# Optimization experiments

Measured on AMD Instinct MI355X. Metric: run time of the kernel, lower is better.

Reference implementation:

```python
import jax, jax.numpy as jnp
import numpy as np
from jax import lax


def _binarize(t):
    # sign binarization to +1/-1 (zero maps to -1, matching torch.where(t > 0, 1, -1))
    return jnp.where(t > 0, 1.0, -1.0).astype(t.dtype)


def _bconv(x, w, b):
    # binary conv: binarize input and weights, then standard 3x3 'same' conv
    y = lax.conv_general_dilated(
        _binarize(x), _binarize(w),
        window_strides=(1, 1), padding=((1, 1), (1, 1)),
        dimension_numbers=('NCHW', 'OIHW', 'NCHW'))
    return y + b[None, :, None, None]


def _maxpool2(x):
    return lax.reduce_window(x, -jnp.inf, lax.max, (1, 1, 2, 2), (1, 1, 2, 2), 'VALID')


def setup_inputs() -> dict:
    key = jax.random.key(0)
    ks = jax.random.split(key, 13)
    s = 0.1
    return {
        'x': jax.random.normal(ks[0], (4096, 1, 28, 28), jnp.float32),
        'w1': jax.random.normal(ks[1], (32, 1, 3, 3), jnp.float32) * s,
        'b1': jax.random.normal(ks[2], (32,), jnp.float32) * s,
        'w2': jax.random.normal(ks[3], (64, 32, 3, 3), jnp.float32) * s,
        'b2': jax.random.normal(ks[4], (64,), jnp.float32) * s,
        'w3': jax.random.normal(ks[5], (16, 64, 3, 3), jnp.float32) * s,
        'b3': jax.random.normal(ks[6], (16,), jnp.float32) * s,
        'fc1_w': jax.random.normal(ks[7], (256, 16 * 7 * 7), jnp.float32) * s,
        'fc1_b': jax.random.normal(ks[8], (256,), jnp.float32) * s,
        'fc2_w': jax.random.normal(ks[9], (128, 256), jnp.float32) * s,
        'fc2_b': jax.random.normal(ks[10], (128,), jnp.float32) * s,
        'fc3_w': jax.random.normal(ks[11], (10, 128), jnp.float32) * s,
        'fc3_b': jax.random.normal(ks[12], (10,), jnp.float32) * s,
    }


def reference(x, w1, b1, w2, b2, w3, b3, fc1_w, fc1_b, fc2_w, fc2_b, fc3_w, fc3_b):
    h = jax.nn.relu(_maxpool2(_bconv(x, w1, b1)))      # [B,32,14,14]
    h = jax.nn.relu(_maxpool2(_bconv(h, w2, b2)))      # [B,64,7,7]
    h = jax.nn.relu(_bconv(h, w3, b3))                 # [B,16,7,7]
    h = h.reshape(-1, 16 * 7 * 7)
    h = jax.nn.relu(h @ fc1_w.T + fc1_b)
    h = jax.nn.relu(h @ fc2_w.T + fc2_b)
    return h @ fc3_w.T + fc3_b                          # [B,10]
```

## Files before the change

kernel.cpp:

```cpp
#include <hip/hip_runtime.h>
#include <cstdint>

#define OFF_W1T   4096
#define OFF_W2T   823296
#define OFF_H3T   954368
#define OFF_H1T   14061568
#define OFF_H2T   18255872

#define TW_WB1    0
#define TW_W2     32
#define TW_W3     608
#define TW_CORR2  896
#define TW_CORR3  1920
#define TW_TLE1   2176
#define TW_TGE1   2208
#define TW_TLE2   2240
#define TW_TGE2   2304

__device__ __forceinline__ int imin2(int a, int b) { return a < b ? a : b; }
__device__ __forceinline__ int imax2(int a, int b) { return a > b ? a : b; }

__device__ __forceinline__ void gload16(const float* g, float* lbase, int lane) {
#if __has_builtin(__builtin_amdgcn_global_load_lds)
    __builtin_amdgcn_global_load_lds(
        (const __attribute__((address_space(1))) uint32_t*)g,
        (__attribute__((address_space(3))) uint32_t*)lbase, 16, 0, 0);
#else
    *(float4*)&lbase[lane * 4] = *(const float4*)g;
#endif
}

__global__ __launch_bounds__(256) void prep(
    const float* __restrict__ w1, const float* __restrict__ b1,
    const float* __restrict__ w2, const float* __restrict__ b2,
    const float* __restrict__ w3,
    const float* __restrict__ fc1_w, const float* __restrict__ fc2_w,
    int* __restrict__ tab, float* __restrict__ w1T, float* __restrict__ w2T) {
    int t = threadIdx.x;
    uint32_t* utab = (uint32_t*)tab;
    if (blockIdx.x == 0) {
        if (t < 32) {
            uint32_t b = 0;
            for (int k = 0; k < 9; ++k) b |= (w1[t * 9 + k] > 0.f ? 1u : 0u) << k;
            utab[TW_WB1 + t] = b;
            tab[TW_TLE1 + t] = (int)floorf((9.f + b1[t]) * 0.5f);
            tab[TW_TGE1 + t] = (int)floorf(-b1[t]) + 1;
        }
        if (t >= 32 && t < 96) {
            int oc = t - 32;
            tab[TW_TLE2 + oc] = (int)floorf((288.f + b2[oc]) * 0.5f);
            tab[TW_TGE2 + oc] = (int)floorf(-b2[oc]) + 1;
        }
        for (int idx = t; idx < 576; idx += 256) {
            int oc = idx / 9, tap = idx % 9;
            int kh = tap / 3, kw = tap % 3;
            uint32_t b = 0;
            for (int ic = 0; ic < 32; ++ic)
                b |= (w2[((oc * 32 + ic) * 3 + kh) * 3 + kw] > 0.f ? 1u : 0u) << ic;
            utab[TW_W2 + idx] = b;
        }
        for (int idx = t; idx < 288; idx += 256) {
            int oc = idx / 18, rem = idx % 18;
            int tap = rem >> 1, word = rem & 1;
            int kh = tap / 3, kw = tap % 3;
            uint32_t b = 0;
            for (int ic = 0; ic < 32; ++ic)
                b |= (w3[((oc * 64 + ic + 32 * word) * 3 + kh) * 3 + kw] > 0.f ? 1u : 0u) << ic;
            utab[TW_W3 + idx] = b;
        }
        __syncthreads();
        for (int idx = t; idx < 1024; idx += 256) {
            int pat = idx >> 6, oc = idx & 63;
            int s = 0, n = 0;
            for (int tap = 0; tap < 9; ++tap) {
                int kh = tap / 3, kw = tap % 3;
                bool pad = ((pat & 1) && kh == 0) || ((pat & 2) && kh == 2) ||
                           ((pat & 4) && kw == 0) || ((pat & 8) && kw == 2);
                if (pad) { s += __popc(utab[TW_W2 + oc * 9 + tap]); ++n; }
            }
            tab[TW_CORR2 + idx] = 2 * s - 32 * n;
        }
        {
            int idx = t;
            if (idx < 256) {
                int pat = idx >> 4, oc = idx & 15;
                int s = 0, n = 0;
                for (int tap = 0; tap < 9; ++tap) {
                    int kh = tap / 3, kw = tap % 3;
                    bool pad = ((pat & 1) && kh == 0) || ((pat & 2) && kh == 2) ||
                               ((pat & 4) && kw == 0) || ((pat & 8) && kw == 2);
                    if (pad) {
                        s += __popc(utab[TW_W3 + oc * 18 + tap * 2]) +
                             __popc(utab[TW_W3 + oc * 18 + tap * 2 + 1]);
                        ++n;
                    }
                }
                tab[TW_CORR3 + idx] = 2 * s - 64 * n;
            }
        }
    } else {
        int e = (blockIdx.x - 1) * 256 + t;
        if (e < 204800) {
            int k = e >> 8, n = e & 255;
            w1T[e] = (k < 784) ? fc1_w[n * 784 + k] : 0.f;
        } else {
            int e2 = e - 204800;
            int k = e2 >> 7, n = e2 & 127;
            w2T[e2] = fc2_w[n * 256 + k];
        }
    }
}

#define WV 456

__global__ __launch_bounds__(512, 8) void conv_stack(
    const float* __restrict__ x,
    const float* __restrict__ b3,
    const int* __restrict__ tab,
    float* __restrict__ h3T) {
    __shared__ int SH[1280 + 4 * WV];
    const int t = threadIdx.x;
    const int wid = t >> 6, lane = t & 63;
    const int iml = wid >> 1, sw = wid & 1;
    const int img = blockIdx.x * 4 + iml;
    const uint32_t* utab = (const uint32_t*)tab;
    uint32_t* W = (uint32_t*)&SH[1280 + iml * WV];

    for (int i = t; i < 1280; i += 512) SH[i] = tab[TW_CORR2 + i];
    for (int i = t; i < 4 * WV; i += 512) SH[1280 + i] = 0;
    __syncthreads();

    if (lane < 14) {
        int r = sw * 14 + lane;
        const float* xr = x + img * 784 + r * 28;
        uint32_t b = 0;
#pragma unroll
        for (int q = 0; q < 7; ++q) {
            float4 v = *(const float4*)(xr + q * 4);
            b |= (v.x > 0.f ? 1u : 0u) << (q * 4 + 0);
            b |= (v.y > 0.f ? 1u : 0u) << (q * 4 + 1);
            b |= (v.z > 0.f ? 1u : 0u) << (q * 4 + 2);
            b |= (v.w > 0.f ? 1u : 0u) << (q * 4 + 3);
        }
        W[1 + r] = b << 1;
    }
    __syncthreads();

    auto conv1_int = [&](int p) {
        int Pi = 1 + p / 12, Pj = 1 + p % 12;
        int i0 = 2 * Pi, j0 = 2 * Pj;
        uint32_t r0 = W[i0], r1 = W[i0 + 1], r2 = W[i0 + 2], r3 = W[i0 + 3];
        uint32_t f0a = (r0 >> j0) & 7, f0b = (r0 >> (j0 + 1)) & 7;
        uint32_t f1a = (r1 >> j0) & 7, f1b = (r1 >> (j0 + 1)) & 7;
        uint32_t f2a = (r2 >> j0) & 7, f2b = (r2 >> (j0 + 1)) & 7;
        uint32_t f3a = (r3 >> j0) & 7, f3b = (r3 >> (j0 + 1)) & 7;
        uint32_t s00 = f0a | (f1a << 3) | (f2a << 6);
        uint32_t s01 = f0b | (f1b << 3) | (f2b << 6);
        uint32_t s10 = f1a | (f2a << 3) | (f3a << 6);
        uint32_t s11 = f1b | (f2b << 3) | (f3b << 6);
        uint32_t word = 0;
#pragma unroll
        for (int oc = 0; oc < 32; ++oc) {
            uint32_t w = utab[TW_WB1 + oc];
            int m0 = __popc(s00 ^ w), m1 = __popc(s01 ^ w);
            int m2 = __popc(s10 ^ w), m3 = __popc(s11 ^ w);
            int mn = imin2(imin2(m0, m1), imin2(m2, m3));
            word |= (mn <= tab[TW_TLE1 + oc] ? 1u : 0u) << oc;
        }
        W[32 + (Pi + 1) * 16 + (Pj + 1)] = word;
    };
    if (sw == 0) {
        conv1_int(lane);
        conv1_int(64 + lane);
    } else {
        if (lane < 16) conv1_int(128 + lane);
        int p = lane;
        bool act = p < 52;
        int pp = act ? p : 28;
        int Pi, Pj;
        if (pp < 14)      { Pi = 0;  Pj = pp; }
        else if (pp < 28) { Pi = 13; Pj = pp - 14; }
        else if (pp < 40) { Pi = pp - 28 + 1; Pj = 0; }
        else              { Pi = pp - 40 + 1; Pj = 13; }
        int i0 = 2 * Pi, j0 = 2 * Pj;
        uint32_t r0 = W[i0], r1 = W[i0 + 1], r2 = W[i0 + 2], r3 = W[i0 + 3];
        uint32_t f0a = (r0 >> j0) & 7, f0b = (r0 >> (j0 + 1)) & 7;
        uint32_t f1a = (r1 >> j0) & 7, f1b = (r1 >> (j0 + 1)) & 7;
        uint32_t f2a = (r2 >> j0) & 7, f2b = (r2 >> (j0 + 1)) & 7;
        uint32_t f3a = (r3 >> j0) & 7, f3b = (r3 >> (j0 + 1)) & 7;
        uint32_t smp[4];
        smp[0] = f0a | (f1a << 3) | (f2a << 6);
        smp[1] = f0b | (f1b << 3) | (f2b << 6);
        smp[2] = f1a | (f2a << 3) | (f3a << 6);
        smp[3] = f1b | (f2b << 3) | (f3b << 6);
        uint32_t mb[4];
        int pcm[4];
#pragma unroll
        for (int a = 0; a < 2; ++a) {
            int i = 2 * Pi + a;
            uint32_t vre = 0x1FF;
            if (i == 0)  vre &= ~0x007u;
            if (i == 27) vre &= ~0x1C0u;
#pragma unroll
            for (int bb = 0; bb < 2; ++bb) {
                int j = 2 * Pj + bb;
                uint32_t vce = 0x1FF;
                if (j == 0)  vce &= ~0x049u;
                if (j == 27) vce &= ~0x124u;
                mb[a * 2 + bb] = vre & vce;
                pcm[a * 2 + bb] = __popc(vre & vce);
            }
        }
        uint32_t word = 0;
#pragma unroll
        for (int oc = 0; oc < 32; ++oc) {
            uint32_t w = utab[TW_WB1 + oc];
            int best = -1000;
#pragma unroll
            for (int p4 = 0; p4 < 4; ++p4) {
                int v = pcm[p4] - 2 * __popc((smp[p4] ^ w) & mb[p4]);
                best = imax2(best, v);
            }
            word |= (best >= tab[TW_TGE1 + oc] ? 1u : 0u) << oc;
        }
        if (act) W[32 + (Pi + 1) * 16 + (Pj + 1)] = word;
    }
    __syncthreads();

    {
        uint32_t w2r[9];
#pragma unroll
        for (int k = 0; k < 9; ++k) w2r[k] = utab[TW_W2 + lane * 9 + k];
        const int tle2 = tab[TW_TLE2 + lane];
        const int tge2 = tab[TW_TGE2 + lane];
        const uint32_t* H1 = W + 32;
        uint32_t* H2 = W + 288;

        for (int q = sw; q < 25; q += 2) {
            int Pi = 1 + q / 5, Pj = 1 + q % 5;
            uint32_t c[16];
#pragma unroll
            for (int r = 0; r < 4; ++r) {
                uint2 lo = *(const uint2*)&H1[(2 * Pi + r) * 16 + 2 * Pj];
                uint2 hi = *(const uint2*)&H1[(2 * Pi + r) * 16 + 2 * Pj + 2];
                c[r * 4 + 0] = lo.x; c[r * 4 + 1] = lo.y;
                c[r * 4 + 2] = hi.x; c[r * 4 + 3] = hi.y;
            }
            int mn = 100000;
#pragma unroll
            for (int a = 0; a < 2; ++a)
#pragma unroll
                for (int bb = 0; bb < 2; ++bb) {
                    int s = 0;
#pragma unroll
                    for (int kh = 0; kh < 3; ++kh)
#pragma unroll
                        for (int kw = 0; kw < 3; ++kw)
                            s += __popc(c[(a + kh) * 4 + (bb + kw)] ^ w2r[kh * 3 + kw]);
                    mn = imin2(mn, s);
                }
            uint64_t bal = __ballot(mn <= tle2);
            if (lane == 0) {
                uint2 wv = make_uint2((uint32_t)bal, (uint32_t)(bal >> 32));
                *(uint2*)&H2[((Pi + 1) * 9 + (Pj + 1)) * 2] = wv;
            }
        }
        for (int bp = sw; bp < 24; bp += 2) {
            int Pi, Pj;
            if (bp < 7)       { Pi = 0; Pj = bp; }
            else if (bp < 14) { Pi = 6; Pj = bp - 7; }
            else if (bp < 19) { Pi = bp - 14 + 1; Pj = 0; }
            else              { Pi = bp - 19 + 1; Pj = 6; }
            uint32_t c[16];
#pragma unroll
            for (int r = 0; r < 4; ++r) {
                uint2 lo = *(const uint2*)&H1[(2 * Pi + r) * 16 + 2 * Pj];
                uint2 hi = *(const uint2*)&H1[(2 * Pi + r) * 16 + 2 * Pj + 2];
                c[r * 4 + 0] = lo.x; c[r * 4 + 1] = lo.y;
                c[r * 4 + 2] = hi.x; c[r * 4 + 3] = hi.y;
            }
            int best = -100000;
#pragma unroll
            for (int a = 0; a < 2; ++a)
#pragma unroll
                for (int bb = 0; bb < 2; ++bb) {
                    int s = 0;
#pragma unroll
                    for (int kh = 0; kh < 3; ++kh)
#pragma unroll
                        for (int kw = 0; kw < 3; ++kw)
                            s += __popc(c[(a + kh) * 4 + (bb + kw)] ^ w2r[kh * 3 + kw]);
                    int i = 2 * Pi + a, j = 2 * Pj + bb;
                    int pat = (i == 0 ? 1 : 0) | (i == 13 ? 2 : 0) |
                              (j == 0 ? 4 : 0) | (j == 13 ? 8 : 0);
                    int D = 288 - 2 * s + SH[pat * 64 + lane];
                    best = imax2(best, D);
                }
            uint64_t bal = __ballot(best >= tge2);
            if (lane == 0) {
                uint2 wv = make_uint2((uint32_t)bal, (uint32_t)(bal >> 32));
                *(uint2*)&H2[((Pi + 1) * 9 + (Pj + 1)) * 2] = wv;
            }
        }
    }
    __syncthreads();

    {
        const uint32_t* H2 = (const uint32_t*)W + 288;
        int oc = lane & 15, sub = lane >> 4;
        uint32_t w3r[18];
#pragma unroll
        for (int k = 0; k < 18; ++k) w3r[k] = utab[TW_W3 + oc * 18 + k];
        float bias3 = b3[oc];
        const int gbeg = sw ? 6 : 0, gend = sw ? 13 : 6;
        for (int g = gbeg; g < gend; ++g) {
            int pos = g * 4 + sub;
            bool act = pos < 49;
            int pp = act ? pos : 0;
            int Pi = pp / 7, Pj = pp % 7;
            int s = 0;
#pragma unroll
            for (int kh = 0; kh < 3; ++kh)
#pragma unroll
                for (int kw = 0; kw < 3; ++kw) {
                    uint2 hv = *(const uint2*)&H2[((Pi + kh) * 9 + (Pj + kw)) * 2];
                    s += __popc(hv.x ^ w3r[(kh * 3 + kw) * 2]) +
                         __popc(hv.y ^ w3r[(kh * 3 + kw) * 2 + 1]);
                }
            int pat = (Pi == 0 ? 1 : 0) | (Pi == 6 ? 2 : 0) |
                      (Pj == 0 ? 4 : 0) | (Pj == 6 ? 8 : 0);
            int D = 576 - 2 * s + SH[1024 + pat * 16 + oc];
            float h = (float)D + bias3;
            h = h > 0.f ? h : 0.f;
            if (act) h3T[(oc * 49 + pp) * 4096 + img] = h;
        }
    }
}

__global__ __launch_bounds__(256) void fc1_gemm(
    const float* __restrict__ aT,
    const float* __restrict__ bT,
    const float* __restrict__ bias,
    float* __restrict__ oT) {
    const int KC = 40;
    __shared__ float As[2][KC * 64];
    __shared__ float Bs[2][KC * 64];
    const int t = threadIdx.x;
    const int lane = t & 63, wid = t >> 6;
    const int tx = t & 15, ty = t >> 4;
    const int img0 = blockIdx.x * 64;
    const int n0 = blockIdx.y * 64;
    float acc[4][4] = {{0.f}};

    auto stage = [&](int buf, int kc) {
        for (int s = wid; s < 20; s += 4) {
            int seg = s < 10 ? s : s - 10;
            int kk = seg * 4 + (lane >> 4);
            int c = (lane & 15) * 4;
            if (s < 10)
                gload16(&aT[(kc + kk) * 4096 + img0 + c], &As[buf][seg * 256], lane);
            else
                gload16(&bT[(kc + kk) * 256 + n0 + c], &Bs[buf][seg * 256], lane);
        }
    };

    stage(0, 0);
    __syncthreads();
    for (int ch = 0; ch < 20; ++ch) {
        int buf = ch & 1;
        if (ch + 1 < 20) stage(buf ^ 1, (ch + 1) * KC);
        const float* A = As[buf];
        const float* B = Bs[buf];
#pragma unroll 8
        for (int kk = 0; kk < KC; ++kk) {
            float4 a = *(const float4*)&A[kk * 64 + ty * 4];
            float4 b = *(const float4*)&B[kk * 64 + tx * 4];
            acc[0][0] += a.x * b.x; acc[0][1] += a.x * b.y;
            acc[0][2] += a.x * b.z; acc[0][3] += a.x * b.w;
            acc[1][0] += a.y * b.x; acc[1][1] += a.y * b.y;
            acc[1][2] += a.y * b.z; acc[1][3] += a.y * b.w;
            acc[2][0] += a.z * b.x; acc[2][1] += a.z * b.y;
            acc[2][2] += a.z * b.z; acc[2][3] += a.z * b.w;
            acc[3][0] += a.w * b.x; acc[3][1] += a.w * b.y;
            acc[3][2] += a.w * b.z; acc[3][3] += a.w * b.w;
        }
        __syncthreads();
    }
    float4 bb = *(const float4*)&bias[n0 + tx * 4];
    float bv[4] = {bb.x, bb.y, bb.z, bb.w};
#pragma unroll
    for (int jj = 0; jj < 4; ++jj) {
        float4 ov;
        ov.x = acc[0][jj] + bv[jj]; ov.x = ov.x > 0.f ? ov.x : 0.f;
        ov.y = acc[1][jj] + bv[jj]; ov.y = ov.y > 0.f ? ov.y : 0.f;
        ov.z = acc[2][jj] + bv[jj]; ov.z = ov.z > 0.f ? ov.z : 0.f;
        ov.w = acc[3][jj] + bv[jj]; ov.w = ov.w > 0.f ? ov.w : 0.f;
        *(float4*)&oT[(n0 + tx * 4 + jj) * 4096 + img0 + ty * 4] = ov;
    }
}

__global__ __launch_bounds__(256) void fc2_gemm(
    const float* __restrict__ aT,
    const float* __restrict__ bT,
    const float* __restrict__ bias,
    float* __restrict__ oT) {
    const int KC = 64;
    __shared__ float As[2][KC * 64];
    __shared__ float Bs[2][KC * 32];
    const int t = threadIdx.x;
    const int lane = t & 63, wid = t >> 6;
    const int tx = t & 15, ty = t >> 4;
    const int img0 = blockIdx.x * 64;
    const int n0 = blockIdx.y * 32;
    float acc[4][2] = {{0.f}};

    auto stage = [&](int buf, int kc) {
        for (int s = wid; s < 24; s += 4) {
            if (s < 16) {
                int kk = s * 4 + (lane >> 4);
                int c = (lane & 15) * 4;
                gload16(&aT[(kc + kk) * 4096 + img0 + c], &As[buf][s * 256], lane);
            } else {
                int seg = s - 16;
                int kk = seg * 8 + (lane >> 3);
                int c = (lane & 7) * 4;
                gload16(&bT[(kc + kk) * 128 + n0 + c], &Bs[buf][seg * 256], lane);
            }
        }
    };

    stage(0, 0);
    __syncthreads();
    for (int ch = 0; ch < 4; ++ch) {
        int buf = ch & 1;
        if (ch + 1 < 4) stage(buf ^ 1, (ch + 1) * KC);
        const float* A = As[buf];
        const float* B = Bs[buf];
#pragma unroll 8
        for (int kk = 0; kk < KC; ++kk) {
            float4 a = *(const float4*)&A[kk * 64 + ty * 4];
            float2 b = *(const float2*)&B[kk * 32 + tx * 2];
            acc[0][0] += a.x * b.x; acc[0][1] += a.x * b.y;
            acc[1][0] += a.y * b.x; acc[1][1] += a.y * b.y;
            acc[2][0] += a.z * b.x; acc[2][1] += a.z * b.y;
            acc[3][0] += a.w * b.x; acc[3][1] += a.w * b.y;
        }
        __syncthreads();
    }
#pragma unroll
    for (int j = 0; j < 2; ++j) {
        int n = n0 + tx * 2 + j;
        float bj = bias[n];
        float4 ov;
        ov.x = acc[0][j] + bj; ov.x = ov.x > 0.f ? ov.x : 0.f;
        ov.y = acc[1][j] + bj; ov.y = ov.y > 0.f ? ov.y : 0.f;
        ov.z = acc[2][j] + bj; ov.z = ov.z > 0.f ? ov.z : 0.f;
        ov.w = acc[3][j] + bj; ov.w = ov.w > 0.f ? ov.w : 0.f;
        *(float4*)&oT[n * 4096 + img0 + ty * 4] = ov;
    }
}

__global__ __launch_bounds__(256) void fc3_gemm(
    const float* __restrict__ aT,
    const float* __restrict__ w,
    const float* __restrict__ bias,
    float* __restrict__ out) {
    int id = blockIdx.x * 256 + threadIdx.x;
    int n = id >> 12, img = id & 4095;
    const float* wr = w + n * 128;
    float a0 = 0.f, a1 = 0.f, a2 = 0.f, a3 = 0.f;
#pragma unroll 8
    for (int k = 0; k < 128; k += 4) {
        a0 += aT[(k + 0) * 4096 + img] * wr[k + 0];
        a1 += aT[(k + 1) * 4096 + img] * wr[k + 1];
        a2 += aT[(k + 2) * 4096 + img] * wr[k + 2];
        a3 += aT[(k + 3) * 4096 + img] * wr[k + 3];
    }
    out[img * 10 + n] = (a0 + a1) + (a2 + a3) + bias[n];
}

extern "C" void kernel_launch(void* const* d_in, const int* in_sizes, int n_in,
                              void* d_out, int out_size, void* d_ws, size_t ws_size,
                              hipStream_t stream) {
    const float* x     = (const float*)d_in[0];
    const float* w1    = (const float*)d_in[1];
    const float* b1    = (const float*)d_in[2];
    const float* w2    = (const float*)d_in[3];
    const float* b2    = (const float*)d_in[4];
    const float* w3    = (const float*)d_in[5];
    const float* b3    = (const float*)d_in[6];
    const float* fc1_w = (const float*)d_in[7];
    const float* fc1_b = (const float*)d_in[8];
    const float* fc2_w = (const float*)d_in[9];
    const float* fc2_b = (const float*)d_in[10];
    const float* fc3_w = (const float*)d_in[11];
    const float* fc3_b = (const float*)d_in[12];
    float* out = (float*)d_out;

    const int B = in_sizes[0] / 784;
    char* ws = (char*)d_ws;
    float* w1T = (float*)(ws + OFF_W1T);
    float* w2T = (float*)(ws + OFF_W2T);
    float* h3T = (float*)(ws + OFF_H3T);
    float* h1T = (float*)(ws + OFF_H1T);
    float* h2T = (float*)(ws + OFF_H2T);
    int* tab = (int*)(ws + OFF_H1T);

    hipLaunchKernelGGL(prep, dim3(929), dim3(256), 0, stream,
                       w1, b1, w2, b2, w3, fc1_w, fc2_w, tab, w1T, w2T);
    hipLaunchKernelGGL(conv_stack, dim3(B / 4), dim3(512), 0, stream,
                       x, b3, tab, h3T);
    hipLaunchKernelGGL(fc1_gemm, dim3(B / 64, 4), dim3(256), 0, stream,
                       h3T, w1T, fc1_b, h1T);
    hipLaunchKernelGGL(fc2_gemm, dim3(B / 64, 4), dim3(256), 0, stream,
                       h1T, w2T, fc2_b, h2T);
    hipLaunchKernelGGL(fc3_gemm, dim3(B * 10 / 256), dim3(256), 0, stream,
                       h2T, fc3_w, fc3_b, out);
}
```

Baseline: 218.4 us.

## Split-K fc1 with atomic accumulation and fuse fc1 bias/ReLU into fc2 load

fc1 now splits K=800 into 8 slices over a third grid dimension. Each 64-thread block computes an 8x8-per-thread 64x64 tile and adds its partial sums atomically into a zeroed h1 buffer. The zeroing is appended to the prep kernel, and fc1 bias+ReLU move into fc2's A-tile staging, so fc2 loads through registers instead of async LDS and loses double buffering. The aim is more blocks and higher register reuse for fc1, at the cost of atomic traffic, an extra zero-fill, and a less pipelined fc2.

```diff
diff --git a/kernel.cpp b/kernel.cpp
--- a/kernel.cpp
+++ b/kernel.cpp
@@ -35,7 +35,8 @@
     const float* __restrict__ w2, const float* __restrict__ b2,
     const float* __restrict__ w3,
     const float* __restrict__ fc1_w, const float* __restrict__ fc2_w,
-    int* __restrict__ tab, float* __restrict__ w1T, float* __restrict__ w2T) {
+    int* __restrict__ tab, float* __restrict__ w1T, float* __restrict__ w2T,
+    float* __restrict__ h1z) {
     int t = threadIdx.x;
     uint32_t* utab = (uint32_t*)tab;
     if (blockIdx.x == 0) {
@@ -98,7 +99,7 @@
                 tab[TW_CORR3 + idx] = 2 * s - 64 * n;
             }
         }
-    } else {
+    } else if (blockIdx.x < 929) {
         int e = (blockIdx.x - 1) * 256 + t;
         if (e < 204800) {
             int k = e >> 8, n = e & 255;
@@ -108,6 +109,9 @@
             int k = e2 >> 7, n = e2 & 127;
             w2T[e2] = fc2_w[n * 256 + k];
         }
+    } else {
+        int e = (blockIdx.x - 929) * 256 + t;
+        *(float4*)&h1z[e * 4] = make_float4(0.f, 0.f, 0.f, 0.f);
     }
 }
 
@@ -337,115 +341,114 @@
     }
 }
 
-__global__ __launch_bounds__(256) void fc1_gemm(
+__global__ __launch_bounds__(64) void fc1_gemm(
     const float* __restrict__ aT,
     const float* __restrict__ bT,
-    const float* __restrict__ bias,
     float* __restrict__ oT) {
-    const int KC = 40;
+    const int KC = 4;
     __shared__ float As[2][KC * 64];
     __shared__ float Bs[2][KC * 64];
     const int t = threadIdx.x;
-    const int lane = t & 63, wid = t >> 6;
-    const int tx = t & 15, ty = t >> 4;
+    const int tx = t & 7, ty = t >> 3;
     const int img0 = blockIdx.x * 64;
     const int n0 = blockIdx.y * 64;
-    float acc[4][4] = {{0.f}};
+    const int k0 = blockIdx.z * 100;
+    float acc[8][8] = {{0.f}};
 
     auto stage = [&](int buf, int kc) {
-        for (int s = wid; s < 20; s += 4) {
-            int seg = s < 10 ? s : s - 10;
-            int kk = seg * 4 + (lane >> 4);
-            int c = (lane & 15) * 4;
-            if (s < 10)
-                gload16(&aT[(kc + kk) * 4096 + img0 + c], &As[buf][seg * 256], lane);
-            else
-                gload16(&bT[(kc + kk) * 256 + n0 + c], &Bs[buf][seg * 256], lane);
-        }
+        int kk = t >> 4, c = (t & 15) * 4;
+        gload16(&aT[(kc + kk) * 4096 + img0 + c], As[buf], t);
+        gload16(&bT[(kc + kk) * 256 + n0 + c], Bs[buf], t);
     };
-
-    stage(0, 0);
-    __syncthreads();
-    for (int ch = 0; ch < 20; ++ch) {
+    stage(0, k0);
+    for (int ch = 0; ch < 25; ++ch) {
         int buf = ch & 1;
-        if (ch + 1 < 20) stage(buf ^ 1, (ch + 1) * KC);
+        if (ch + 1 < 25) {
+            stage(buf ^ 1, k0 + (ch + 1) * KC);
+            asm volatile("s_waitcnt vmcnt(2)" ::: "memory");
+        } else {
+            asm volatile("s_waitcnt vmcnt(0)" ::: "memory");
+        }
         const float* A = As[buf];
         const float* B = Bs[buf];
-#pragma unroll 8
+#pragma unroll
         for (int kk = 0; kk < KC; ++kk) {
-            float4 a = *(const float4*)&A[kk * 64 + ty * 4];
-            float4 b = *(const float4*)&B[kk * 64 + tx * 4];
-            acc[0][0] += a.x * b.x; acc[0][1] += a.x * b.y;
-            acc[0][2] += a.x * b.z; acc[0][3] += a.x * b.w;
-            acc[1][0] += a.y * b.x; acc[1][1] += a.y * b.y;
-            acc[1][2] += a.y * b.z; acc[1][3] += a.y * b.w;
-            acc[2][0] += a.z * b.x; acc[2][1] += a.z * b.y;
-            acc[2][2] += a.z * b.z; acc[2][3] += a.z * b.w;
-            acc[3][0] += a.w * b.x; acc[3][1] += a.w * b.y;
-            acc[3][2] += a.w * b.z; acc[3][3] += a.w * b.w;
-        }
-        __syncthreads();
-    }
-    float4 bb = *(const float4*)&bias[n0 + tx * 4];
-    float bv[4] = {bb.x, bb.y, bb.z, bb.w};
-#pragma unroll
-    for (int jj = 0; jj < 4; ++jj) {
-        float4 ov;
-        ov.x = acc[0][jj] + bv[jj]; ov.x = ov.x > 0.f ? ov.x : 0.f;
-        ov.y = acc[1][jj] + bv[jj]; ov.y = ov.y > 0.f ? ov.y : 0.f;
-        ov.z = acc[2][jj] + bv[jj]; ov.z = ov.z > 0.f ? ov.z : 0.f;
-        ov.w = acc[3][jj] + bv[jj]; ov.w = ov.w > 0.f ? ov.w : 0.f;
-        *(float4*)&oT[(n0 + tx * 4 + jj) * 4096 + img0 + ty * 4] = ov;
-    }
+            float4 a0 = *(const float4*)&A[kk * 64 + ty * 8];
+            float4 a1 = *(const float4*)&A[kk * 64 + ty * 8 + 4];
+            float4 b0 = *(const float4*)&B[kk * 64 + tx * 8];
+            float4 b1 = *(const float4*)&B[kk * 64 + tx * 8 + 4];
+            float av[8] = {a0.x, a0.y, a0.z, a0.w, a1.x, a1.y, a1.z, a1.w};
+            float bv[8] = {b0.x, b0.y, b0.z, b0.w, b1.x, b1.y, b1.z, b1.w};
+#pragma unroll
+            for (int i = 0; i < 8; ++i)
+#pragma unroll
+                for (int j = 0; j < 8; ++j)
+                    acc[i][j] += av[i] * bv[j];
+        }
+    }
+#pragma unroll
+    for (int i = 0; i < 8; ++i)
+#pragma unroll
+        for (int j = 0; j < 8; ++j)
+            unsafeAtomicAdd(&oT[(n0 + tx * 8 + j) * 4096 + img0 + ty * 8 + i],
+                            acc[i][j]);
 }
 
 __global__ __launch_bounds__(256) void fc2_gemm(
     const float* __restrict__ aT,
     const float* __restrict__ bT,
+    const float* __restrict__ b1v,
     const float* __restrict__ bias,
     float* __restrict__ oT) {
     const int KC = 64;
-    __shared__ float As[2][KC * 64];
-    __shared__ float Bs[2][KC * 32];
+    __shared__ float As[KC * 64];
+    __shared__ float Bs[KC * 32];
+    __shared__ float sb[256];
     const int t = threadIdx.x;
-    const int lane = t & 63, wid = t >> 6;
+    const int wid = t >> 6;
     const int tx = t & 15, ty = t >> 4;
     const int img0 = blockIdx.x * 64;
     const int n0 = blockIdx.y * 32;
     float acc[4][2] = {{0.f}};
 
-    auto stage = [&](int buf, int kc) {
-        for (int s = wid; s < 24; s += 4) {
-            if (s < 16) {
-                int kk = s * 4 + (lane >> 4);
-                int c = (lane & 15) * 4;
-                gload16(&aT[(kc + kk) * 4096 + img0 + c], &As[buf][s * 256], lane);
-            } else {
-                int seg = s - 16;
-                int kk = seg * 8 + (lane >> 3);
-                int c = (lane & 7) * 4;
-                gload16(&bT[(kc + kk) * 128 + n0 + c], &Bs[buf][seg * 256], lane);
-            }
-        }
-    };
-
-    stage(0, 0);
+    sb[t] = b1v[t];
     __syncthreads();
+
     for (int ch = 0; ch < 4; ++ch) {
-        int buf = ch & 1;
-        if (ch + 1 < 4) stage(buf ^ 1, (ch + 1) * KC);
-        const float* A = As[buf];
-        const float* B = Bs[buf];
+        int kc = ch * KC;
+        float4 xa[4]; float ba[4];
+#pragma unroll
+        for (int s = 0; s < 4; ++s) {
+            int v = t + s * 256, kk = v >> 4, c = (v & 15) * 4;
+            xa[s] = *(const float4*)&aT[(kc + kk) * 4096 + img0 + c];
+            ba[s] = sb[kc + kk];
+        }
+        __syncthreads();
+#pragma unroll
+        for (int s = 0; s < 4; ++s) {
+            int v = t + s * 256, kk = v >> 4, c = (v & 15) * 4;
+            float4 x = xa[s]; float bb = ba[s];
+            x.x = fmaxf(x.x + bb, 0.f); x.y = fmaxf(x.y + bb, 0.f);
+            x.z = fmaxf(x.z + bb, 0.f); x.w = fmaxf(x.w + bb, 0.f);
+            *(float4*)&As[kk * 64 + c] = x;
+        }
+#pragma unroll
+        for (int s = 0; s < 2; ++s) {
+            int seg = wid + s * 4;
+            int v = seg * 64 + (t & 63);
+            int kk = v >> 3, c = (v & 7) * 4;
+            gload16(&bT[(kc + kk) * 128 + n0 + c], &Bs[seg * 256], t & 63);
+        }
+        __syncthreads();
 #pragma unroll 8
         for (int kk = 0; kk < KC; ++kk) {
-            float4 a = *(const float4*)&A[kk * 64 + ty * 4];
-            float2 b = *(const float2*)&B[kk * 32 + tx * 2];
+            float4 a = *(const float4*)&As[kk * 64 + ty * 4];
+            float2 b = *(const float2*)&Bs[kk * 32 + tx * 2];
             acc[0][0] += a.x * b.x; acc[0][1] += a.x * b.y;
             acc[1][0] += a.y * b.x; acc[1][1] += a.y * b.y;
             acc[2][0] += a.z * b.x; acc[2][1] += a.z * b.y;
             acc[3][0] += a.w * b.x; acc[3][1] += a.w * b.y;
         }
-        __syncthreads();
     }
 #pragma unroll
     for (int j = 0; j < 2; ++j) {
@@ -504,16 +507,16 @@
     float* h3T = (float*)(ws + OFF_H3T);
     float* h1T = (float*)(ws + OFF_H1T);
     float* h2T = (float*)(ws + OFF_H2T);
-    int* tab = (int*)(ws + OFF_H1T);
-
-    hipLaunchKernelGGL(prep, dim3(929), dim3(256), 0, stream,
-                       w1, b1, w2, b2, w3, fc1_w, fc2_w, tab, w1T, w2T);
+    int* tab = (int*)(ws + OFF_H2T);
+
+    hipLaunchKernelGGL(prep, dim3(1953), dim3(256), 0, stream,
+                       w1, b1, w2, b2, w3, fc1_w, fc2_w, tab, w1T, w2T, h1T);
     hipLaunchKernelGGL(conv_stack, dim3(B / 4), dim3(512), 0, stream,
                        x, b3, tab, h3T);
-    hipLaunchKernelGGL(fc1_gemm, dim3(B / 64, 4), dim3(256), 0, stream,
-                       h3T, w1T, fc1_b, h1T);
+    hipLaunchKernelGGL(fc1_gemm, dim3(B / 64, 4, 8), dim3(64), 0, stream,
+                       h3T, w1T, h1T);
     hipLaunchKernelGGL(fc2_gemm, dim3(B / 64, 4), dim3(256), 0, stream,
-                       h1T, w2T, fc2_b, h2T);
+                       h1T, w2T, fc1_b, fc2_b, h2T);
     hipLaunchKernelGGL(fc3_gemm, dim3(B * 10 / 256), dim3(256), 0, stream,
                        h2T, fc3_w, fc3_b, out);
 }
```

New measurement: 400.6 us. 1.83x slower.

## Replace LDS-tiled FC GEMMs with per-wave register GEMMs and tile weight transposes

Applied to the files above, without the earlier changes.

The fc1 and fc2 GEMMs no longer stage A and B tiles into LDS with double buffering. Each lane now owns one image, and each wave reads a uniform row of B (wave-broadcast float4 loads) while accumulating 16 or 8 outputs in registers, which removes LDS traffic and barriers. The prep kernel now transposes the fc1 and fc2 weights through shared-memory 64x64 tiles instead of strided per-element gathers, cutting its grid from 929 blocks to 61. The lookup table moves to the h2T workspace region. Per-thread reuse drops to one A value per k, so arithmetic intensity falls and the GEMMs lean more on cache for the B reads.

```diff
diff --git a/kernel.cpp b/kernel.cpp
--- a/kernel.cpp
+++ b/kernel.cpp
@@ -19,16 +19,6 @@
 
 __device__ __forceinline__ int imin2(int a, int b) { return a < b ? a : b; }
 __device__ __forceinline__ int imax2(int a, int b) { return a > b ? a : b; }
-
-__device__ __forceinline__ void gload16(const float* g, float* lbase, int lane) {
-#if __has_builtin(__builtin_amdgcn_global_load_lds)
-    __builtin_amdgcn_global_load_lds(
-        (const __attribute__((address_space(1))) uint32_t*)g,
-        (__attribute__((address_space(3))) uint32_t*)lbase, 16, 0, 0);
-#else
-    *(float4*)&lbase[lane * 4] = *(const float4*)g;
-#endif
-}
 
 __global__ __launch_bounds__(256) void prep(
     const float* __restrict__ w1, const float* __restrict__ b1,
@@ -80,33 +70,56 @@
             }
             tab[TW_CORR2 + idx] = 2 * s - 32 * n;
         }
-        {
-            int idx = t;
-            if (idx < 256) {
-                int pat = idx >> 4, oc = idx & 15;
-                int s = 0, n = 0;
-                for (int tap = 0; tap < 9; ++tap) {
-                    int kh = tap / 3, kw = tap % 3;
-                    bool pad = ((pat & 1) && kh == 0) || ((pat & 2) && kh == 2) ||
-                               ((pat & 4) && kw == 0) || ((pat & 8) && kw == 2);
-                    if (pad) {
-                        s += __popc(utab[TW_W3 + oc * 18 + tap * 2]) +
-                             __popc(utab[TW_W3 + oc * 18 + tap * 2 + 1]);
-                        ++n;
-                    }
+        if (t < 256) {
+            int pat = t >> 4, oc = t & 15;
+            int s = 0, n = 0;
+            for (int tap = 0; tap < 9; ++tap) {
+                int kh = tap / 3, kw = tap % 3;
+                bool pad = ((pat & 1) && kh == 0) || ((pat & 2) && kh == 2) ||
+                           ((pat & 4) && kw == 0) || ((pat & 8) && kw == 2);
+                if (pad) {
+                    s += __popc(utab[TW_W3 + oc * 18 + tap * 2]) +
+                         __popc(utab[TW_W3 + oc * 18 + tap * 2 + 1]);
+                    ++n;
                 }
-                tab[TW_CORR3 + idx] = 2 * s - 64 * n;
-            }
+            }
+            tab[TW_CORR3 + t] = 2 * s - 64 * n;
+        }
+    } else if (blockIdx.x <= 52) {
+        __shared__ float T[64][65];
+        int bb = blockIdx.x - 1;
+        int kt = bb >> 2, nt = bb & 3;
+#pragma unroll
+        for (int s = 0; s < 16; ++s) {
+            int idx = s * 256 + t;
+            int nl = idx >> 6, kl = idx & 63;
+            int k = kt * 64 + kl;
+            T[nl][kl] = (k < 784) ? fc1_w[(nt * 64 + nl) * 784 + k] : 0.f;
+        }
+        __syncthreads();
+#pragma unroll
+        for (int s = 0; s < 16; ++s) {
+            int idx = s * 256 + t;
+            int kl = idx >> 6, nl = idx & 63;
+            int k = kt * 64 + kl;
+            if (k < 800) w1T[k * 256 + nt * 64 + nl] = T[nl][kl];
         }
     } else {
-        int e = (blockIdx.x - 1) * 256 + t;
-        if (e < 204800) {
-            int k = e >> 8, n = e & 255;
-            w1T[e] = (k < 784) ? fc1_w[n * 784 + k] : 0.f;
-        } else {
-            int e2 = e - 204800;
-            int k = e2 >> 7, n = e2 & 127;
-            w2T[e2] = fc2_w[n * 256 + k];
+        __shared__ float T[64][65];
+        int bb = blockIdx.x - 53;
+        int kt = bb >> 1, nt = bb & 1;
+#pragma unroll
+        for (int s = 0; s < 16; ++s) {
+            int idx = s * 256 + t;
+            int nl = idx >> 6, kl = idx & 63;
+            T[nl][kl] = fc2_w[(nt * 64 + nl) * 256 + kt * 64 + kl];
+        }
+        __syncthreads();
+#pragma unroll
+        for (int s = 0; s < 16; ++s) {
+            int idx = s * 256 + t;
+            int kl = idx >> 6, nl = idx & 63;
+            w2T[(kt * 64 + kl) * 128 + nt * 64 + nl] = T[nl][kl];
         }
     }
 }
@@ -342,60 +355,36 @@
     const float* __restrict__ bT,
     const float* __restrict__ bias,
     float* __restrict__ oT) {
-    const int KC = 40;
-    __shared__ float As[2][KC * 64];
-    __shared__ float Bs[2][KC * 64];
     const int t = threadIdx.x;
-    const int lane = t & 63, wid = t >> 6;
-    const int tx = t & 15, ty = t >> 4;
-    const int img0 = blockIdx.x * 64;
-    const int n0 = blockIdx.y * 64;
-    float acc[4][4] = {{0.f}};
-
-    auto stage = [&](int buf, int kc) {
-        for (int s = wid; s < 20; s += 4) {
-            int seg = s < 10 ? s : s - 10;
-            int kk = seg * 4 + (lane >> 4);
-            int c = (lane & 15) * 4;
-            if (s < 10)
-                gload16(&aT[(kc + kk) * 4096 + img0 + c], &As[buf][seg * 256], lane);
-            else
-                gload16(&bT[(kc + kk) * 256 + n0 + c], &Bs[buf][seg * 256], lane);
-        }
-    };
-
-    stage(0, 0);
-    __syncthreads();
-    for (int ch = 0; ch < 20; ++ch) {
-        int buf = ch & 1;
-        if (ch + 1 < 20) stage(buf ^ 1, (ch + 1) * KC);
-        const float* A = As[buf];
-        const float* B = Bs[buf];
+    const int lane = t & 63;
+    const int wu = __builtin_amdgcn_readfirstlane(t >> 6);
+    const int img = blockIdx.x * 64 + lane;
+    const int nw = blockIdx.y * 64 + wu * 16;
+    const float* __restrict__ Ac = aT + img;
+    const float* __restrict__ Bc = bT + nw;
+    float acc[16];
+#pragma unroll
+    for (int j = 0; j < 16; ++j) acc[j] = 0.f;
+
 #pragma unroll 8
-        for (int kk = 0; kk < KC; ++kk) {
-            float4 a = *(const float4*)&A[kk * 64 + ty * 4];
-            float4 b = *(const float4*)&B[kk * 64 + tx * 4];
-            acc[0][0] += a.x * b.x; acc[0][1] += a.x * b.y;
-            acc[0][2] += a.x * b.z; acc[0][3] += a.x * b.w;
-            acc[1][0] += a.y * b.x; acc[1][1] += a.y * b.y;
-            acc[1][2] += a.y * b.z; acc[1][3] += a.y * b.w;
-            acc[2][0] += a.z * b.x; acc[2][1] += a.z * b.y;
-            acc[2][2] += a.z * b.z; acc[2][3] += a.z * b.w;
-            acc[3][0] += a.w * b.x; acc[3][1] += a.w * b.y;
-            acc[3][2] += a.w * b.z; acc[3][3] += a.w * b.w;
-        }
-        __syncthreads();
-    }
-    float4 bb = *(const float4*)&bias[n0 + tx * 4];
-    float bv[4] = {bb.x, bb.y, bb.z, bb.w};
-#pragma unroll
-    for (int jj = 0; jj < 4; ++jj) {
-        float4 ov;
-        ov.x = acc[0][jj] + bv[jj]; ov.x = ov.x > 0.f ? ov.x : 0.f;
-        ov.y = acc[1][jj] + bv[jj]; ov.y = ov.y > 0.f ? ov.y : 0.f;
-        ov.z = acc[2][jj] + bv[jj]; ov.z = ov.z > 0.f ? ov.z : 0.f;
-        ov.w = acc[3][jj] + bv[jj]; ov.w = ov.w > 0.f ? ov.w : 0.f;
-        *(float4*)&oT[(n0 + tx * 4 + jj) * 4096 + img0 + ty * 4] = ov;
+    for (int k = 0; k < 800; ++k) {
+        float a = Ac[k * 4096];
+        const float4* B4 = (const float4*)(Bc + k * 256);
+        float4 b0 = B4[0], b1 = B4[1], b2 = B4[2], b3 = B4[3];
+        acc[0]  += a * b0.x; acc[1]  += a * b0.y;
+        acc[2]  += a * b0.z; acc[3]  += a * b0.w;
+        acc[4]  += a * b1.x; acc[5]  += a * b1.y;
+        acc[6]  += a * b1.z; acc[7]  += a * b1.w;
+        acc[8]  += a * b2.x; acc[9]  += a * b2.y;
+        acc[10] += a * b2.z; acc[11] += a * b2.w;
+        acc[12] += a * b3.x; acc[13] += a * b3.y;
+        acc[14] += a * b3.z; acc[15] += a * b3.w;
+    }
+#pragma unroll
+    for (int j = 0; j < 16; ++j) {
+        float v = acc[j] + bias[nw + j];
+        v = v > 0.f ? v : 0.f;
+        oT[(nw + j) * 4096 + img] = v;
     }
 }
 
@@ -404,59 +393,32 @@
     const float* __restrict__ bT,
     const float* __restrict__ bias,
     float* __restrict__ oT) {
-    const int KC = 64;
-    __shared__ float As[2][KC * 64];
-    __shared__ float Bs[2][KC * 32];
     const int t = threadIdx.x;
-    const int lane = t & 63, wid = t >> 6;
-    const int tx = t & 15, ty = t >> 4;
-    const int img0 = blockIdx.x * 64;
-    const int n0 = blockIdx.y * 32;
-    float acc[4][2] = {{0.f}};
-
-    auto stage = [&](int buf, int kc) {
-        for (int s = wid; s < 24; s += 4) {
-            if (s < 16) {
-                int kk = s * 4 + (lane >> 4);
-                int c = (lane & 15) * 4;
-                gload16(&aT[(kc + kk) * 4096 + img0 + c], &As[buf][s * 256], lane);
-            } else {
-                int seg = s - 16;
-                int kk = seg * 8 + (lane >> 3);
-                int c = (lane & 7) * 4;
-                gload16(&bT[(kc + kk) * 128 + n0 + c], &Bs[buf][seg * 256], lane);
-            }
-        }
-    };
-
-    stage(0, 0);
-    __syncthreads();
-    for (int ch = 0; ch < 4; ++ch) {
-        int buf = ch & 1;
-        if (ch + 1 < 4) stage(buf ^ 1, (ch + 1) * KC);
-        const float* A = As[buf];
-        const float* B = Bs[buf];
+    const int lane = t & 63;
+    const int wu = __builtin_amdgcn_readfirstlane(t >> 6);
+    const int img = blockIdx.x * 64 + lane;
+    const int nw = blockIdx.y * 32 + wu * 8;
+    const float* __restrict__ Ac = aT + img;
+    const float* __restrict__ Bc = bT + nw;
+    float acc[8];
+#pragma unroll
+    for (int j = 0; j < 8; ++j) acc[j] = 0.f;
+
 #pragma unroll 8
-        for (int kk = 0; kk < KC; ++kk) {
-            float4 a = *(const float4*)&A[kk * 64 + ty * 4];
-            float2 b = *(const float2*)&B[kk * 32 + tx * 2];
-            acc[0][0] += a.x * b.x; acc[0][1] += a.x * b.y;
-            acc[1][0] += a.y * b.x; acc[1][1] += a.y * b.y;
-            acc[2][0] += a.z * b.x; acc[2][1] += a.z * b.y;
-            acc[3][0] += a.w * b.x; acc[3][1] += a.w * b.y;
-        }
-        __syncthreads();
-    }
-#pragma unroll
-    for (int j = 0; j < 2; ++j) {
-        int n = n0 + tx * 2 + j;
-        float bj = bias[n];
-        float4 ov;
-        ov.x = acc[0][j] + bj; ov.x = ov.x > 0.f ? ov.x : 0.f;
-        ov.y = acc[1][j] + bj; ov.y = ov.y > 0.f ? ov.y : 0.f;
-        ov.z = acc[2][j] + bj; ov.z = ov.z > 0.f ? ov.z : 0.f;
-        ov.w = acc[3][j] + bj; ov.w = ov.w > 0.f ? ov.w : 0.f;
-        *(float4*)&oT[n * 4096 + img0 + ty * 4] = ov;
+    for (int k = 0; k < 256; ++k) {
+        float a = Ac[k * 4096];
+        const float4* B4 = (const float4*)(Bc + k * 128);
+        float4 b0 = B4[0], b1 = B4[1];
+        acc[0] += a * b0.x; acc[1] += a * b0.y;
+        acc[2] += a * b0.z; acc[3] += a * b0.w;
+        acc[4] += a * b1.x; acc[5] += a * b1.y;
+        acc[6] += a * b1.z; acc[7] += a * b1.w;
+    }
+#pragma unroll
+    for (int j = 0; j < 8; ++j) {
+        float v = acc[j] + bias[nw + j];
+        v = v > 0.f ? v : 0.f;
+        oT[(nw + j) * 4096 + img] = v;
     }
 }
 
@@ -504,9 +466,9 @@
     float* h3T = (float*)(ws + OFF_H3T);
     float* h1T = (float*)(ws + OFF_H1T);
     float* h2T = (float*)(ws + OFF_H2T);
-    int* tab = (int*)(ws + OFF_H1T);
-
-    hipLaunchKernelGGL(prep, dim3(929), dim3(256), 0, stream,
+    int* tab = (int*)(ws + OFF_H2T);
+
+    hipLaunchKernelGGL(prep, dim3(61), dim3(256), 0, stream,
                        w1, b1, w2, b2, w3, fc1_w, fc2_w, tab, w1T, w2T);
     hipLaunchKernelGGL(conv_stack, dim3(B / 4), dim3(512), 0, stream,
                        x, b3, tab, h3T);
```

Measured after the change: 279.8 us. 28.2% more time.
